# Performance work log

Measured on AMD Instinct MI355X. Metric: run time of the kernel, lower is better.

Reference implementation:

```python
import jax, jax.numpy as jnp
import numpy as np

BN_EPS = 1e-5
L2_EPS = 1e-12

def _conv2d(x, w, pad):
    # x: NCHW, w: OIHW
    return jax.lax.conv_general_dilated(
        x, w, window_strides=(1, 1), padding=[(pad, pad), (pad, pad)],
        dimension_numbers=('NCHW', 'OIHW', 'NCHW'))

def _l2norm(x, axis):
    n = jnp.sqrt(jnp.sum(x * x, axis=axis, keepdims=True))
    return x / jnp.maximum(n, L2_EPS)

def setup_inputs() -> dict:
    key = jax.random.key(0)
    ks = jax.random.split(key, 8)
    x = jax.random.normal(ks[0], (16, 512, 32, 32), dtype=jnp.float32)
    w_proj1 = jax.random.normal(ks[1], (512, 512, 3, 3), dtype=jnp.float32) * 0.02
    bn_gamma = jnp.ones((512,), dtype=jnp.float32)
    bn_beta = jnp.zeros((512,), dtype=jnp.float32)
    bn_mean = jnp.zeros((512,), dtype=jnp.float32)
    bn_var = jnp.ones((512,), dtype=jnp.float32)
    w_proj2 = jax.random.normal(ks[2], (512, 512, 3, 3), dtype=jnp.float32) * 0.02
    w_assign = jax.random.normal(ks[3], (64, 512, 1, 1), dtype=jnp.float32)
    centroids = jax.random.uniform(ks[4], (64, 512), dtype=jnp.float32)
    return {'x': x, 'w_proj1': w_proj1, 'bn_gamma': bn_gamma, 'bn_beta': bn_beta,
            'bn_mean': bn_mean, 'bn_var': bn_var, 'w_proj2': w_proj2,
            'w_assign': w_assign, 'centroids': centroids}

def reference(x, w_proj1, bn_gamma, bn_beta, bn_mean, bn_var, w_proj2, w_assign, centroids):
    # projection head: conv3x3 -> BN (eval) -> ReLU -> conv3x3
    h = _conv2d(x, w_proj1, pad=1)
    inv = jax.lax.rsqrt(bn_var + BN_EPS)
    h = (h - bn_mean[None, :, None, None]) * (bn_gamma * inv)[None, :, None, None] + bn_beta[None, :, None, None]
    h = jax.nn.relu(h)
    x_enc = _conv2d(h, w_proj2, pad=1)

    # descriptor-wise L2 normalization over channels
    xn = _l2norm(x_enc, axis=1)
    N, C, H, W = xn.shape
    K = w_assign.shape[0]

    # soft assignment: 1x1 conv -> softmax over clusters
    sa = _conv2d(xn, w_assign, pad=0).reshape(N, K, H * W)  # [N,K,L]
    sa = jax.nn.softmax(sa, axis=1)

    xf = xn.reshape(N, C, H * W)  # [N,C,L]
    # algebraic rewrite of the per-cluster residual loop:
    # vlad[n,k,c] = sum_l sa[n,k,l]*(xf[n,c,l] - cent[k,c])
    vlad = jnp.einsum('nkl,ncl->nkc', sa, xf) - sa.sum(-1)[:, :, None] * centroids[None]
    vlad = _l2norm(vlad, axis=2)          # intra-normalization
    vlad = vlad.reshape(N, K * C)
    vlad = _l2norm(vlad, axis=1)          # global L2 norm
    return (vlad, x_enc)
```

## Files before the change

kernel.cpp:

```cpp
#include <hip/hip_runtime.h>
#include <math.h>


typedef __bf16 bf16x8 __attribute__((ext_vector_type(8)));
typedef float f32x4 __attribute__((ext_vector_type(4)));

#define GLDS16(gp, lp)                                                  \
  __builtin_amdgcn_global_load_lds(                                     \
      (const __attribute__((address_space(1))) void*)(gp),              \
      (__attribute__((address_space(3))) void*)(lp), 16, 0, 0)

template <int MODE>
__global__ __launch_bounds__(256) void conv_gemm(
    const __bf16* __restrict__ in,
    const __bf16* __restrict__ wt,
    const float* __restrict__ scale, const float* __restrict__ shift,
    __bf16* __restrict__ outp) {
  __shared__ __align__(16) __bf16 Hl[6 * 42 * 64];
  __shared__ __align__(16) __bf16 Wl[2 * 128 * 64];

  const int t = threadIdx.x;
  const int bx = blockIdx.x, oT = blockIdx.y;
  const int lane = t & 63, wid = t >> 6;
  const int l16 = lane & 15, q = lane >> 4;
  const int wrow = wid >> 1, wcol = wid & 1;

  const int n = bx >> 3;
  const int trow0 = (bx & 7) * 4;

  const int swr = t >> 3, sp = t & 7;
  const __bf16* wsrc[4];
#pragma unroll
  for (int i = 0; i < 4; ++i)
    wsrc[i] = wt + (size_t)(oT * 128 + 32 * i + swr) * 4608 + sp * 8;

  const __bf16* inb = in + (size_t)n * (1156 * 512);
  const __bf16* hsrc[8];
  bool hval[8];
#pragma unroll
  for (int i = 0; i < 8; ++i) {
    const int jj = t + 256 * i;
    hval[i] = jj < 2016;
    const int hr = jj / 336;
    const int hrem = jj - hr * 336;
    const int hw = hrem >> 3, hc8 = hrem & 7;
    hsrc[i] = inb + ((size_t)((trow0 + hr) * 34 + hw)) * 512 +
              (hc8 ^ (hw & 7)) * 8;
  }

  const int c0 = (q ^ (l16 & 7)) * 8;
  const int c1 = ((4 + q) ^ (l16 & 7)) * 8;
  int aoff[4], prow_[4], pcol_[4];
#pragma unroll
  for (int i = 0; i < 4; ++i) {
    aoff[i] = (wrow * 64 + i * 16 + l16) * 64;
    const int p = wcol * 64 + i * 16 + l16;
    prow_[i] = p >> 5;
    pcol_[i] = p & 31;
  }

  f32x4 acc[4][4];
#pragma unroll
  for (int i = 0; i < 4; ++i)
#pragma unroll
    for (int j = 0; j < 4; ++j) acc[i][j] = (f32x4){0.f, 0.f, 0.f, 0.f};

#pragma unroll
  for (int i = 0; i < 8; ++i)
    if (hval[i]) GLDS16(hsrc[i], Hl + (t + 256 * i) * 8);
#pragma unroll
  for (int i = 0; i < 4; ++i)
    GLDS16(wsrc[i], Wl + (t + 256 * i) * 8);
#pragma unroll
  for (int i = 0; i < 4; ++i)
    GLDS16(wsrc[i] + 512, Wl + 8192 + (t + 256 * i) * 8);
  asm volatile("s_waitcnt vmcnt(4)" ::: "memory");
  __builtin_amdgcn_s_barrier();

  int tap = 0, dh = 0, dw = 0, cc = 0;
  int tap2 = 2, cc2 = 0;

#pragma unroll 1
  for (int s = 0; s < 72; ++s) {
    const int buf = (s & 1) << 13;
    const __bf16* Wb = Wl + buf;

    bf16x8 aw[4][2], bp[4][2];
#pragma unroll
    for (int i = 0; i < 4; ++i) {
      aw[i][0] = *(const bf16x8*)&Wb[aoff[i] + c0];
      aw[i][1] = *(const bf16x8*)&Wb[aoff[i] + c1];
    }
#pragma unroll
    for (int i = 0; i < 4; ++i) {
      const int col = pcol_[i] + dw;
      const int rb = (prow_[i] + dh) * 2688 + col * 64;
      const int xr = col & 7;
      bp[i][0] = *(const bf16x8*)&Hl[rb + (q ^ xr) * 8];
      bp[i][1] = *(const bf16x8*)&Hl[rb + ((4 + q) ^ xr) * 8];
    }
    asm volatile("s_waitcnt lgkmcnt(0)" ::: "memory");
    __builtin_amdgcn_sched_barrier(0);
    __builtin_amdgcn_s_barrier();

    if (tap == 8 && cc < 7) {
#pragma unroll
      for (int i = 0; i < 8; ++i)
        if (hval[i]) GLDS16(hsrc[i] + (cc + 1) * 64, Hl + (t + 256 * i) * 8);
    }
    if (s < 70) {
      const int woffs2 = (tap2 * 8 + cc2) * 64;
#pragma unroll
      for (int i = 0; i < 4; ++i)
        GLDS16(wsrc[i] + woffs2, Wl + buf + (t + 256 * i) * 8);
    }

    __builtin_amdgcn_s_setprio(1);
#pragma unroll
    for (int kh = 0; kh < 2; ++kh)
#pragma unroll
      for (int mt = 0; mt < 4; ++mt)
#pragma unroll
        for (int nt = 0; nt < 4; ++nt)
          acc[mt][nt] = __builtin_amdgcn_mfma_f32_16x16x32_bf16(
              aw[mt][kh], bp[nt][kh], acc[mt][nt], 0, 0, 0);
    __builtin_amdgcn_s_setprio(0);

    if (s < 70)
      asm volatile("s_waitcnt vmcnt(4)" ::: "memory");
    else
      asm volatile("s_waitcnt vmcnt(0)" ::: "memory");
    __builtin_amdgcn_s_barrier();

    ++tap;
    ++dw;
    if (dw == 3) {
      dw = 0;
      ++dh;
    }
    if (tap == 9) {
      tap = 0;
      dh = 0;
      dw = 0;
      ++cc;
    }
    if (++tap2 == 9) {
      tap2 = 0;
      ++cc2;
    }
  }

#pragma unroll
  for (int nt = 0; nt < 4; ++nt) {
    const int m_l = wcol * 64 + nt * 16 + l16;
    const int mg2 = bx * 128 + m_l;
    const int n2 = mg2 >> 10, pix2 = mg2 & 1023;
#pragma unroll
    for (int mt = 0; mt < 4; ++mt) {
      const int ob = oT * 128 + wrow * 64 + mt * 16 + q * 4;
      f32x4 v = acc[mt][nt];
      union {
        __bf16 b[4];
        uint2 u;
      } pk;
      if (MODE == 0) {
        const f32x4 sc = *(const f32x4*)&scale[ob];
        const f32x4 sh = *(const f32x4*)&shift[ob];
#pragma unroll
        for (int r = 0; r < 4; ++r)
          pk.b[r] = (__bf16)fmaxf(v[r] * sc[r] + sh[r], 0.f);
        __bf16* dst = outp +
                      ((size_t)n2 * 1156 + ((pix2 >> 5) + 1) * 34 +
                       ((pix2 & 31) + 1)) * 512 + ob;
        *(uint2*)dst = pk.u;
      } else {
#pragma unroll
        for (int r = 0; r < 4; ++r) pk.b[r] = (__bf16)v[r];
        __bf16* dst = outp + ((size_t)n2 * 1024 + pix2) * 512 + ob;
        *(uint2*)dst = pk.u;
      }
    }
  }
}

__global__ __launch_bounds__(256) void expand_x(const __bf16* __restrict__ xebT,
                                                float* __restrict__ xenc,
                                                __bf16* __restrict__ xeb) {
  __shared__ __align__(16) __bf16 Ll[64 * 64];
  const int t = threadIdx.x;
  const int cc = blockIdx.x, ptile = blockIdx.y, n = blockIdx.z;
  const int p0 = ptile * 64, c0 = cc * 64;
#pragma unroll
  for (int i = 0; i < 2; ++i) {
    const int u = t * 2 + i;
    const int pix = u >> 3, c8 = u & 7;
    uint4 v =
        *(const uint4*)&xebT[((size_t)n * 1024 + p0 + pix) * 512 + c0 + c8 * 8];
    *(uint4*)&Ll[pix * 64 + (c8 ^ (pix & 7)) * 8] = v;
  }
  __syncthreads();
  const int c = t >> 2, g = t & 3;
  union {
    float f[4];
    float4 v;
  } fv[4];
  union {
    __bf16 b[16];
    uint4 u[2];
  } bv;
#pragma unroll
  for (int r = 0; r < 16; ++r) {
    const int pix = g * 16 + r;
    __bf16 b = Ll[pix * 64 + ((c >> 3) ^ (pix & 7)) * 8 + (c & 7)];
    bv.b[r] = b;
    fv[r >> 2].f[r & 3] = (float)b;
  }
  float* fd = xenc + ((size_t)n * 512 + c0 + c) * 1024 + p0 + g * 16;
#pragma unroll
  for (int r = 0; r < 4; ++r) *(float4*)(fd + r * 4) = fv[r].v;
  __bf16* bd = xeb + ((size_t)n * 512 + c0 + c) * 1024 + p0 + g * 16;
  *(uint4*)bd = bv.u[0];
  *(uint4*)(bd + 8) = bv.u[1];
}

__global__ __launch_bounds__(256) void assign_softmax(
    const __bf16* __restrict__ xebT, const __bf16* __restrict__ watb,
    __bf16* __restrict__ saPb, float* __restrict__ S) {
  __shared__ __align__(16) __bf16 Al[4][64 * 32];
  __shared__ __align__(16) __bf16 Wlb[4][64 * 32];
  __shared__ float Sl[64];
  const int t = threadIdx.x;
  const int pt = blockIdx.x, n = blockIdx.y;
  const int lane = t & 63, wid = t >> 6;
  const int l16 = lane & 15, q = lane >> 4;
  if (t < 64) Sl[t] = 0.f;

  const int arow = t >> 2;
  const __bf16* asrc = xebT + ((size_t)n * 1024 + pt * 64 + arow) * 512 +
                       ((t & 3) ^ ((arow >> 1) & 3)) * 8;
  const __bf16* wsrc = watb + (size_t)(t >> 2) * 512 + (t & 3) * 8;
  const int ldsb = wid * 512;
  const int sw = (q ^ ((l16 >> 1) & 3)) * 8;
  const int pnoff = (t >> 2) * 32 + (t & 3) * 8;

  f32x4 acc[4];
#pragma unroll
  for (int i = 0; i < 4; ++i) acc[i] = (f32x4){0.f, 0.f, 0.f, 0.f};
  float pn = 0.f;

#pragma unroll
  for (int p = 0; p < 3; ++p) {
    GLDS16(asrc + p * 32, (__bf16*)Al[p] + ldsb);
    GLDS16(wsrc + p * 32, (__bf16*)Wlb[p] + ldsb);
  }
  asm volatile("s_waitcnt vmcnt(4)" ::: "memory");
  __builtin_amdgcn_s_barrier();

#pragma unroll 1
  for (int kc = 0; kc < 16; ++kc) {
    const __bf16* Ab = Al[kc & 3];
    const __bf16* Wb = Wlb[kc & 3];
    bf16x8 pv = *(const bf16x8*)&Ab[pnoff];
    bf16x8 pf = *(const bf16x8*)&Ab[(wid * 16 + l16) * 32 + sw];
    bf16x8 wf[4];
#pragma unroll
    for (int ka = 0; ka < 4; ++ka)
      wf[ka] = *(const bf16x8*)&Wb[(ka * 16 + l16) * 32 + sw];
    asm volatile("s_waitcnt lgkmcnt(0)" ::: "memory");
    __builtin_amdgcn_sched_barrier(0);
    __builtin_amdgcn_s_barrier();
    if (kc + 3 < 16) {
      GLDS16(asrc + (kc + 3) * 32, (__bf16*)Al[(kc + 3) & 3] + ldsb);
      GLDS16(wsrc + (kc + 3) * 32, (__bf16*)Wlb[(kc + 3) & 3] + ldsb);
    }
#pragma unroll
    for (int j = 0; j < 8; ++j) {
      float f = (float)pv[j];
      pn = fmaf(f, f, pn);
    }
#pragma unroll
    for (int ka = 0; ka < 4; ++ka)
      acc[ka] =
          __builtin_amdgcn_mfma_f32_16x16x32_bf16(wf[ka], pf, acc[ka], 0, 0, 0);
    if (kc < 13)
      asm volatile("s_waitcnt vmcnt(4)" ::: "memory");
    else
      asm volatile("s_waitcnt vmcnt(0)" ::: "memory");
    __builtin_amdgcn_s_barrier();
  }
  pn += __shfl_xor(pn, 1);
  pn += __shfl_xor(pn, 2);
  const float rn = 1.0f / fmaxf(sqrtf(__shfl(pn, l16 * 4)), 1e-12f);

  float sc[16];
  float m = -3.4e38f;
#pragma unroll
  for (int ka = 0; ka < 4; ++ka)
#pragma unroll
    for (int r = 0; r < 4; ++r) {
      float v = acc[ka][r] * rn;
      sc[ka * 4 + r] = v;
      m = fmaxf(m, v);
    }
  m = fmaxf(m, __shfl_xor(m, 16));
  m = fmaxf(m, __shfl_xor(m, 32));
  float s = 0.f;
#pragma unroll
  for (int j = 0; j < 16; ++j) {
    sc[j] = __expf(sc[j] - m);
    s += sc[j];
  }
  s += __shfl_xor(s, 16);
  s += __shfl_xor(s, 32);
  const float inv = 1.0f / s;
  const int pixg = pt * 64 + wid * 16 + l16;
#pragma unroll
  for (int j = 0; j < 16; ++j) {
    const int k = (j >> 2) * 16 + q * 4 + (j & 3);
    float sa = sc[j] * inv;
    sc[j] = sa;
    saPb[((size_t)n * 64 + k) * 1024 + pixg] = (__bf16)(sa * rn);
  }
#pragma unroll
  for (int j = 0; j < 16; ++j) {
    float v = sc[j];
    v += __shfl_xor(v, 1);
    v += __shfl_xor(v, 2);
    v += __shfl_xor(v, 4);
    v += __shfl_xor(v, 8);
    sc[j] = v;
  }
  if (l16 == 0) {
#pragma unroll
    for (int j = 0; j < 16; ++j)
      atomicAdd(&Sl[(j >> 2) * 16 + q * 4 + (j & 3)], sc[j]);
  }
  __syncthreads();
  if (t < 64) atomicAdd(&S[n * 64 + t], Sl[t]);
}

__global__ __launch_bounds__(256) void vlad_gemm(
    const __bf16* __restrict__ saPb, const __bf16* __restrict__ xeb,
    float* __restrict__ vpart) {
  __shared__ __align__(16) __bf16 Al[4][64 * 32];
  __shared__ __align__(16) __bf16 Bl[4][128 * 32];

  const int t = threadIdx.x;
  const int cT = blockIdx.x, n = blockIdx.y, ks = blockIdx.z;
  const int lane = t & 63, wid = t >> 6;
  const int l16 = lane & 15, q = lane >> 4;
  const int wrow = wid >> 1, wcol = wid & 1;

  const int ar = t >> 2, acp = t & 3;
  const __bf16* asrc = saPb + (size_t)n * 65536 + (size_t)ar * 1024 + ks * 256 +
                       (acp ^ ((ar >> 1) & 3)) * 8;
  const int br0 = t >> 2, bcp0 = t & 3;
  const int br1 = (t + 256) >> 2, bcp1 = t & 3;
  const __bf16* bsrc0 = xeb + (size_t)n * 524288 +
                        (size_t)(cT * 128 + br0) * 1024 + ks * 256 +
                        (bcp0 ^ ((br0 >> 1) & 3)) * 8;
  const __bf16* bsrc1 = xeb + (size_t)n * 524288 +
                        (size_t)(cT * 128 + br1) * 1024 + ks * 256 +
                        (bcp1 ^ ((br1 >> 1) & 3)) * 8;

  const int ldsb = wid * 512;
  const int sw = (q ^ ((l16 >> 1) & 3)) * 8;

  f32x4 acc[2][4];
#pragma unroll
  for (int i = 0; i < 2; ++i)
#pragma unroll
    for (int j = 0; j < 4; ++j) acc[i][j] = (f32x4){0.f, 0.f, 0.f, 0.f};

#pragma unroll
  for (int p = 0; p < 3; ++p) {
    GLDS16(asrc + p * 32, (__bf16*)Al[p] + ldsb);
    GLDS16(bsrc0 + p * 32, (__bf16*)Bl[p] + ldsb);
    GLDS16(bsrc1 + p * 32, (__bf16*)Bl[p] + 2048 + ldsb);
  }
  asm volatile("s_waitcnt vmcnt(6)" ::: "memory");
  __builtin_amdgcn_s_barrier();

#pragma unroll 1
  for (int kc = 0; kc < 8; ++kc) {
    const __bf16* Ab = Al[kc & 3];
    const __bf16* Bb = Bl[kc & 3];
    bf16x8 af[2], bf[4];
#pragma unroll
    for (int i = 0; i < 2; ++i)
      af[i] = *(const bf16x8*)&Ab[(wrow * 32 + i * 16 + l16) * 32 + sw];
#pragma unroll
    for (int i = 0; i < 4; ++i)
      bf[i] = *(const bf16x8*)&Bb[(wcol * 64 + i * 16 + l16) * 32 + sw];
    asm volatile("s_waitcnt lgkmcnt(0)" ::: "memory");
    __builtin_amdgcn_sched_barrier(0);
    __builtin_amdgcn_s_barrier();
    if (kc + 3 < 8) {
      GLDS16(asrc + (kc + 3) * 32, (__bf16*)Al[(kc + 3) & 3] + ldsb);
      GLDS16(bsrc0 + (kc + 3) * 32, (__bf16*)Bl[(kc + 3) & 3] + ldsb);
      GLDS16(bsrc1 + (kc + 3) * 32, (__bf16*)Bl[(kc + 3) & 3] + 2048 + ldsb);
    }
#pragma unroll
    for (int mt = 0; mt < 2; ++mt)
#pragma unroll
      for (int nt = 0; nt < 4; ++nt)
        acc[mt][nt] = __builtin_amdgcn_mfma_f32_16x16x32_bf16(
            af[mt], bf[nt], acc[mt][nt], 0, 0, 0);
    if (kc < 5)
      asm volatile("s_waitcnt vmcnt(6)" ::: "memory");
    else
      asm volatile("s_waitcnt vmcnt(0)" ::: "memory");
    __builtin_amdgcn_s_barrier();
  }

  float* vp = vpart + (size_t)(ks * 16 + n) * 32768;
#pragma unroll
  for (int mt = 0; mt < 2; ++mt) {
    const int krow = wrow * 32 + mt * 16 + q * 4;
#pragma unroll
    for (int nt = 0; nt < 4; ++nt) {
      const int ccol = cT * 128 + wcol * 64 + nt * 16 + l16;
#pragma unroll
      for (int r = 0; r < 4; ++r)
        vp[(size_t)(krow + r) * 512 + ccol] = acc[mt][nt][r];
    }
  }
}

__global__ __launch_bounds__(64) void intra_norm(float* __restrict__ vraw,
                                                 const float* __restrict__ vpart,
                                                 const float* __restrict__ S,
                                                 const float* __restrict__ cent,
                                                 float* __restrict__ gss) {
  const int b = blockIdx.x;
  const int n = b >> 6, k = b & 63;
  const int lane = threadIdx.x;
  const float s = S[b];
  float v[8];
  float ss = 0.f;
#pragma unroll
  for (int j = 0; j < 8; ++j) {
    const int c = lane * 8 + j;
    const size_t off = (size_t)b * 512 + c;
    float val = vpart[off] + vpart[524288 + off] + vpart[2 * 524288 + off] +
                vpart[3 * 524288 + off] - s * cent[k * 512 + c];
    v[j] = val;
    ss += val * val;
  }
#pragma unroll
  for (int off = 1; off < 64; off <<= 1) ss += __shfl_xor(ss, off);
  const float rn = 1.0f / fmaxf(sqrtf(ss), 1e-12f);
#pragma unroll
  for (int j = 0; j < 8; ++j) vraw[(size_t)b * 512 + lane * 8 + j] = v[j] * rn;
  if (lane == 0) atomicAdd(&gss[n], ss * rn * rn);
}

__global__ __launch_bounds__(256) void finalize(const float* __restrict__ vraw,
                                                const float* __restrict__ gss,
                                                float* __restrict__ out) {
  const int id = blockIdx.x * 256 + threadIdx.x;
  const int n = id >> 15;
  out[id] = vraw[id] * (1.0f / fmaxf(sqrtf(gss[n]), 1e-12f));
}

__global__ __launch_bounds__(256) void prep_all(
    const float* __restrict__ x, const float* __restrict__ w1,
    const float* __restrict__ w2, const float* __restrict__ g,
    const float* __restrict__ b, const float* __restrict__ m,
    const float* __restrict__ v, const float* __restrict__ wA,
    __bf16* __restrict__ xpad, __bf16* __restrict__ hpad,
    __bf16* __restrict__ wt1, __bf16* __restrict__ wt2,
    float* __restrict__ scale, float* __restrict__ shift,
    __bf16* __restrict__ watb, float* __restrict__ Sz) {
  __shared__ float Lw[4608];
  const int bx = blockIdx.x;
  const int t = threadIdx.x;

  if (bx < 1056) {
    const int which = bx >= 528;
    const int id = (which ? bx - 528 : bx) * 256 + t;
    const int n = id / 8448;
    const int rem = id - n * 8448;
    const int pb = rem >> 6;
    const int c8 = rem & 63;
    int h, w;
    if (pb < 34) {
      h = 0;
      w = pb;
    } else if (pb < 68) {
      h = 33;
      w = pb - 34;
    } else {
      const int r2 = pb - 68;
      h = 1 + (r2 >> 1);
      w = (r2 & 1) * 33;
    }
    __bf16* base = which ? hpad : xpad;
    *(uint4*)(base + ((size_t)n * 1156 + h * 34 + w) * 512 + c8 * 8) =
        (uint4){0u, 0u, 0u, 0u};
  } else if (bx < 1191) {
    const int i = (bx - 1056) * 256 + t;
    if (i < 512) {
      float sc = g[i] / sqrtf(v[i] + 1e-5f);
      scale[i] = sc;
      shift[i] = b[i] - m[i] * sc;
    } else if (i < 512 + 32768) {
      const int id = i - 512;
      const int k = id >> 9, j = id & 511;
      const int kt = j >> 5, cpos = (j >> 3) & 3, e = j & 7;
      const int c = kt * 32 + (cpos ^ ((k >> 1) & 3)) * 8 + e;
      watb[(size_t)k * 512 + j] = (__bf16)wA[(size_t)k * 512 + c];
    } else if (i < 512 + 32768 + 1040) {
      Sz[i - (512 + 32768)] = 0.f;
    }
  } else if (bx < 1703) {
    const int bb = bx - 1191;
    const int n = bb >> 5, h = bb & 31;
    const int w = t & 31, cg = t >> 5;
    const float* src = x + ((size_t)n * 512 + cg * 64) * 1024 + h * 32 + w;
    __bf16* dst =
        xpad + ((size_t)n * 1156 + (h + 1) * 34 + (w + 1)) * 512 + cg * 64;
    float fv[64];
#pragma unroll
    for (int j = 0; j < 64; ++j) fv[j] = src[j * 1024];
#pragma unroll
    for (int jj = 0; jj < 8; ++jj) {
      union {
        __bf16 b8[8];
        uint4 u;
      } pk;
#pragma unroll
      for (int j = 0; j < 8; ++j) pk.b8[j] = (__bf16)fv[jj * 8 + j];
      *(uint4*)(dst + jj * 8) = pk.u;
    }
  } else {
    const int bb = bx - 1703;
    const int o = bb & 511;
    const float* w = (bb >> 9) ? w2 : w1;
    __bf16* wt = (bb >> 9) ? wt2 : wt1;
#pragma unroll
    for (int i = 0; i < 18; ++i)
      Lw[t + 256 * i] = w[(size_t)o * 4608 + t + 256 * i];
    __syncthreads();
#pragma unroll
    for (int i = 0; i < 18; ++i) {
      const int idk = t + 256 * i;
      const int kt = idk >> 6;
      const int p = (idk >> 3) & 7, e = idk & 7;
      const int logical = p ^ (o & 7);
      const int k2 = kt * 64 + logical * 8 + e;
      const int tap = k2 >> 9, ci = k2 & 511;
      wt[(size_t)o * 4608 + idk] = (__bf16)Lw[ci * 9 + tap];
    }
  }
}

extern "C" void kernel_launch(void* const* d_in, const int* in_sizes, int n_in,
                              void* d_out, int out_size, void* d_ws,
                              size_t ws_size, hipStream_t stream) {
  const float* x = (const float*)d_in[0];
  const float* w1 = (const float*)d_in[1];
  const float* gam = (const float*)d_in[2];
  const float* bet = (const float*)d_in[3];
  const float* mean = (const float*)d_in[4];
  const float* var = (const float*)d_in[5];
  const float* w2 = (const float*)d_in[6];
  const float* wA = (const float*)d_in[7];
  const float* cent = (const float*)d_in[8];
  float* out = (float*)d_out;

  char* ws = (char*)d_ws;
  __bf16* Wt1 = (__bf16*)(ws + 0);
  __bf16* Wt2 = (__bf16*)(ws + 4718592);
  __bf16* xpad = (__bf16*)(ws + 9437184);
  __bf16* xebT = (__bf16*)(ws + 9437184);
  __bf16* saPb = (__bf16*)(ws + 26214400);
  __bf16* hpad = (__bf16*)(ws + 28377088);
  __bf16* xeb = (__bf16*)(ws + 28377088);
  float* vpart = (float*)(ws + 0);
  float* vraw = (float*)(ws + 8388608);
  float* scale = (float*)(ws + 47316992);
  float* shift = (float*)(ws + 47319040);
  __bf16* watb = (__bf16*)(ws + 47321088);
  float* S = (float*)(ws + 47386624);
  float* gss = (float*)(ws + 47390720);

  float* xenc = out + 524288;

  prep_all<<<2727, 256, 0, stream>>>(x, w1, w2, gam, bet, mean, var, wA, xpad,
                                     hpad, Wt1, Wt2, scale, shift, watb, S);

  conv_gemm<0><<<dim3(128, 4), 256, 0, stream>>>(xpad, Wt1, scale, shift, hpad);
  conv_gemm<1><<<dim3(128, 4), 256, 0, stream>>>(hpad, Wt2, nullptr, nullptr,
                                                 xebT);

  expand_x<<<dim3(8, 16, 16), 256, 0, stream>>>(xebT, xenc, xeb);
  assign_softmax<<<dim3(16, 16), 256, 0, stream>>>(xebT, watb, saPb, S);
  vlad_gemm<<<dim3(4, 16, 4), 256, 0, stream>>>(saPb, xeb, vpart);
  intra_norm<<<1024, 64, 0, stream>>>(vraw, vpart, S, cent, gss);
  finalize<<<2048, 256, 0, stream>>>(vraw, gss, out);
}
```

Baseline: 309.6 us.

## Fuse channel-major x_enc output into conv epilogue and split MFMA k-halves

Removes the expand_x kernel: the second conv's epilogue now also writes the fp32 x_enc and bf16 channel-major copies directly, using strided scalar stores. The inner loop is also restructured so the first k-half of MFMAs runs before the LDS barrier, overlapping compute with the remaining LDS reads and the barrier wait. This saves a kernel launch and a global read of xebT, but the epilogue scatter stores are uncoalesced and may cost bandwidth.

```diff
diff --git a/kernel.cpp b/kernel.cpp
--- a/kernel.cpp
+++ b/kernel.cpp
@@ -15,7 +15,8 @@
     const __bf16* __restrict__ in,
     const __bf16* __restrict__ wt,
     const float* __restrict__ scale, const float* __restrict__ shift,
-    __bf16* __restrict__ outp) {
+    __bf16* __restrict__ outp, float* __restrict__ xenc,
+    __bf16* __restrict__ xeb) {
   __shared__ __align__(16) __bf16 Hl[6 * 42 * 64];
   __shared__ __align__(16) __bf16 Wl[2 * 128 * 64];
 
@@ -85,20 +86,32 @@
     const int buf = (s & 1) << 13;
     const __bf16* Wb = Wl + buf;
 
-    bf16x8 aw[4][2], bp[4][2];
-#pragma unroll
-    for (int i = 0; i < 4; ++i) {
-      aw[i][0] = *(const bf16x8*)&Wb[aoff[i] + c0];
-      aw[i][1] = *(const bf16x8*)&Wb[aoff[i] + c1];
-    }
+    bf16x8 aw0[4], aw1[4], bp0[4], bp1[4];
+    int rbs[4], xrs[4];
+#pragma unroll
+    for (int i = 0; i < 4; ++i) aw0[i] = *(const bf16x8*)&Wb[aoff[i] + c0];
 #pragma unroll
     for (int i = 0; i < 4; ++i) {
       const int col = pcol_[i] + dw;
-      const int rb = (prow_[i] + dh) * 2688 + col * 64;
-      const int xr = col & 7;
-      bp[i][0] = *(const bf16x8*)&Hl[rb + (q ^ xr) * 8];
-      bp[i][1] = *(const bf16x8*)&Hl[rb + ((4 + q) ^ xr) * 8];
-    }
+      rbs[i] = (prow_[i] + dh) * 2688 + col * 64;
+      xrs[i] = col & 7;
+      bp0[i] = *(const bf16x8*)&Hl[rbs[i] + (q ^ xrs[i]) * 8];
+    }
+#pragma unroll
+    for (int i = 0; i < 4; ++i) aw1[i] = *(const bf16x8*)&Wb[aoff[i] + c1];
+#pragma unroll
+    for (int i = 0; i < 4; ++i)
+      bp1[i] = *(const bf16x8*)&Hl[rbs[i] + ((4 + q) ^ xrs[i]) * 8];
+
+    __builtin_amdgcn_s_setprio(1);
+#pragma unroll
+    for (int mt = 0; mt < 4; ++mt)
+#pragma unroll
+      for (int nt = 0; nt < 4; ++nt)
+        acc[mt][nt] = __builtin_amdgcn_mfma_f32_16x16x32_bf16(
+            aw0[mt], bp0[nt], acc[mt][nt], 0, 0, 0);
+    __builtin_amdgcn_s_setprio(0);
+
     asm volatile("s_waitcnt lgkmcnt(0)" ::: "memory");
     __builtin_amdgcn_sched_barrier(0);
     __builtin_amdgcn_s_barrier();
@@ -117,13 +130,11 @@
 
     __builtin_amdgcn_s_setprio(1);
 #pragma unroll
-    for (int kh = 0; kh < 2; ++kh)
-#pragma unroll
-      for (int mt = 0; mt < 4; ++mt)
-#pragma unroll
-        for (int nt = 0; nt < 4; ++nt)
-          acc[mt][nt] = __builtin_amdgcn_mfma_f32_16x16x32_bf16(
-              aw[mt][kh], bp[nt][kh], acc[mt][nt], 0, 0, 0);
+    for (int mt = 0; mt < 4; ++mt)
+#pragma unroll
+      for (int nt = 0; nt < 4; ++nt)
+        acc[mt][nt] = __builtin_amdgcn_mfma_f32_16x16x32_bf16(
+            aw1[mt], bp1[nt], acc[mt][nt], 0, 0, 0);
     __builtin_amdgcn_s_setprio(0);
 
     if (s < 70)
@@ -178,49 +189,15 @@
         for (int r = 0; r < 4; ++r) pk.b[r] = (__bf16)v[r];
         __bf16* dst = outp + ((size_t)n2 * 1024 + pix2) * 512 + ob;
         *(uint2*)dst = pk.u;
+        const size_t cb = ((size_t)n2 * 512 + ob) * 1024 + pix2;
+#pragma unroll
+        for (int r = 0; r < 4; ++r) {
+          xenc[cb + (size_t)r * 1024] = v[r];
+          xeb[cb + (size_t)r * 1024] = pk.b[r];
+        }
       }
     }
   }
-}
-
-__global__ __launch_bounds__(256) void expand_x(const __bf16* __restrict__ xebT,
-                                                float* __restrict__ xenc,
-                                                __bf16* __restrict__ xeb) {
-  __shared__ __align__(16) __bf16 Ll[64 * 64];
-  const int t = threadIdx.x;
-  const int cc = blockIdx.x, ptile = blockIdx.y, n = blockIdx.z;
-  const int p0 = ptile * 64, c0 = cc * 64;
-#pragma unroll
-  for (int i = 0; i < 2; ++i) {
-    const int u = t * 2 + i;
-    const int pix = u >> 3, c8 = u & 7;
-    uint4 v =
-        *(const uint4*)&xebT[((size_t)n * 1024 + p0 + pix) * 512 + c0 + c8 * 8];
-    *(uint4*)&Ll[pix * 64 + (c8 ^ (pix & 7)) * 8] = v;
-  }
-  __syncthreads();
-  const int c = t >> 2, g = t & 3;
-  union {
-    float f[4];
-    float4 v;
-  } fv[4];
-  union {
-    __bf16 b[16];
-    uint4 u[2];
-  } bv;
-#pragma unroll
-  for (int r = 0; r < 16; ++r) {
-    const int pix = g * 16 + r;
-    __bf16 b = Ll[pix * 64 + ((c >> 3) ^ (pix & 7)) * 8 + (c & 7)];
-    bv.b[r] = b;
-    fv[r >> 2].f[r & 3] = (float)b;
-  }
-  float* fd = xenc + ((size_t)n * 512 + c0 + c) * 1024 + p0 + g * 16;
-#pragma unroll
-  for (int r = 0; r < 4; ++r) *(float4*)(fd + r * 4) = fv[r].v;
-  __bf16* bd = xeb + ((size_t)n * 512 + c0 + c) * 1024 + p0 + g * 16;
-  *(uint4*)bd = bv.u[0];
-  *(uint4*)(bd + 8) = bv.u[1];
 }
 
 __global__ __launch_bounds__(256) void assign_softmax(
@@ -590,11 +567,11 @@
   prep_all<<<2727, 256, 0, stream>>>(x, w1, w2, gam, bet, mean, var, wA, xpad,
                                      hpad, Wt1, Wt2, scale, shift, watb, S);
 
-  conv_gemm<0><<<dim3(128, 4), 256, 0, stream>>>(xpad, Wt1, scale, shift, hpad);
+  conv_gemm<0><<<dim3(128, 4), 256, 0, stream>>>(xpad, Wt1, scale, shift, hpad,
+                                                 nullptr, nullptr);
   conv_gemm<1><<<dim3(128, 4), 256, 0, stream>>>(hpad, Wt2, nullptr, nullptr,
-                                                 xebT);
-
-  expand_x<<<dim3(8, 16, 16), 256, 0, stream>>>(xebT, xenc, xeb);
+                                                 xebT, xenc, xeb);
+
   assign_softmax<<<dim3(16, 16), 256, 0, stream>>>(xebT, watb, saPb, S);
   vlad_gemm<<<dim3(4, 16, 4), 256, 0, stream>>>(saPb, xeb, vpart);
   intra_norm<<<1024, 64, 0, stream>>>(vraw, vpart, S, cent, gss);
```

New measurement: 319.9 us. 3.3% more time.

## Triple-buffer conv weight tiles, split MFMA k-halves, merge post-conv kernels

Applied to the files above, without the earlier changes.

The conv GEMM main loop now rotates weight tiles through three LDS buffers instead of two. This drops the per-step LDS-read barrier except when the input tile is refilled, and each step's MFMAs are split into two k-halves so the first half can start while the second half's fragments are still loading. Separately, expand_x and assign_softmax are merged into one launch that branches on block index, saving a launch and letting the two run concurrently. The cost is more LDS per block for the conv, which may cut occupancy, and a larger shared-memory footprint for the merged kernel's transpose blocks.

```diff
diff --git a/kernel.cpp b/kernel.cpp
--- a/kernel.cpp
+++ b/kernel.cpp
@@ -17,7 +17,7 @@
     const float* __restrict__ scale, const float* __restrict__ shift,
     __bf16* __restrict__ outp) {
   __shared__ __align__(16) __bf16 Hl[6 * 42 * 64];
-  __shared__ __align__(16) __bf16 Wl[2 * 128 * 64];
+  __shared__ __align__(16) __bf16 Wl[3 * 128 * 64];
 
   const int t = threadIdx.x;
   const int bx = blockIdx.x, oT = blockIdx.y;
@@ -79,51 +79,64 @@
 
   int tap = 0, dh = 0, dw = 0, cc = 0;
   int tap2 = 2, cc2 = 0;
+  int cur = 0;
 
 #pragma unroll 1
   for (int s = 0; s < 72; ++s) {
-    const int buf = (s & 1) << 13;
-    const __bf16* Wb = Wl + buf;
-
-    bf16x8 aw[4][2], bp[4][2];
-#pragma unroll
-    for (int i = 0; i < 4; ++i) {
-      aw[i][0] = *(const bf16x8*)&Wb[aoff[i] + c0];
-      aw[i][1] = *(const bf16x8*)&Wb[aoff[i] + c1];
-    }
+    const __bf16* Wb = Wl + cur * 8192;
+
+    bf16x8 aw0[4], aw1[4], bp0[4], bp1[4];
+    int rbs[4], xrs[4];
+#pragma unroll
+    for (int i = 0; i < 4; ++i) aw0[i] = *(const bf16x8*)&Wb[aoff[i] + c0];
 #pragma unroll
     for (int i = 0; i < 4; ++i) {
       const int col = pcol_[i] + dw;
-      const int rb = (prow_[i] + dh) * 2688 + col * 64;
-      const int xr = col & 7;
-      bp[i][0] = *(const bf16x8*)&Hl[rb + (q ^ xr) * 8];
-      bp[i][1] = *(const bf16x8*)&Hl[rb + ((4 + q) ^ xr) * 8];
-    }
-    asm volatile("s_waitcnt lgkmcnt(0)" ::: "memory");
-    __builtin_amdgcn_sched_barrier(0);
-    __builtin_amdgcn_s_barrier();
-
-    if (tap == 8 && cc < 7) {
-#pragma unroll
-      for (int i = 0; i < 8; ++i)
-        if (hval[i]) GLDS16(hsrc[i] + (cc + 1) * 64, Hl + (t + 256 * i) * 8);
+      rbs[i] = (prow_[i] + dh) * 2688 + col * 64;
+      xrs[i] = col & 7;
+      bp0[i] = *(const bf16x8*)&Hl[rbs[i] + (q ^ xrs[i]) * 8];
+    }
+#pragma unroll
+    for (int i = 0; i < 4; ++i) aw1[i] = *(const bf16x8*)&Wb[aoff[i] + c1];
+#pragma unroll
+    for (int i = 0; i < 4; ++i)
+      bp1[i] = *(const bf16x8*)&Hl[rbs[i] + ((4 + q) ^ xrs[i]) * 8];
+
+    __builtin_amdgcn_s_setprio(1);
+#pragma unroll
+    for (int mt = 0; mt < 4; ++mt)
+#pragma unroll
+      for (int nt = 0; nt < 4; ++nt)
+        acc[mt][nt] = __builtin_amdgcn_mfma_f32_16x16x32_bf16(
+            aw0[mt], bp0[nt], acc[mt][nt], 0, 0, 0);
+    __builtin_amdgcn_s_setprio(0);
+
+    if (tap == 8) {
+      asm volatile("s_waitcnt lgkmcnt(0)" ::: "memory");
+      __builtin_amdgcn_sched_barrier(0);
+      __builtin_amdgcn_s_barrier();
+      if (cc < 7) {
+#pragma unroll
+        for (int i = 0; i < 8; ++i)
+          if (hval[i]) GLDS16(hsrc[i] + (cc + 1) * 64, Hl + (t + 256 * i) * 8);
+      }
     }
     if (s < 70) {
+      int b2 = cur + 2;
+      if (b2 >= 3) b2 -= 3;
       const int woffs2 = (tap2 * 8 + cc2) * 64;
 #pragma unroll
       for (int i = 0; i < 4; ++i)
-        GLDS16(wsrc[i] + woffs2, Wl + buf + (t + 256 * i) * 8);
+        GLDS16(wsrc[i] + woffs2, Wl + b2 * 8192 + (t + 256 * i) * 8);
     }
 
     __builtin_amdgcn_s_setprio(1);
 #pragma unroll
-    for (int kh = 0; kh < 2; ++kh)
-#pragma unroll
-      for (int mt = 0; mt < 4; ++mt)
-#pragma unroll
-        for (int nt = 0; nt < 4; ++nt)
-          acc[mt][nt] = __builtin_amdgcn_mfma_f32_16x16x32_bf16(
-              aw[mt][kh], bp[nt][kh], acc[mt][nt], 0, 0, 0);
+    for (int mt = 0; mt < 4; ++mt)
+#pragma unroll
+      for (int nt = 0; nt < 4; ++nt)
+        acc[mt][nt] = __builtin_amdgcn_mfma_f32_16x16x32_bf16(
+            aw1[mt], bp1[nt], acc[mt][nt], 0, 0, 0);
     __builtin_amdgcn_s_setprio(0);
 
     if (s < 70)
@@ -148,6 +161,7 @@
       tap2 = 0;
       ++cc2;
     }
+    if (++cur == 3) cur = 0;
   }
 
 #pragma unroll
@@ -183,160 +197,161 @@
   }
 }
 
-__global__ __launch_bounds__(256) void expand_x(const __bf16* __restrict__ xebT,
-                                                float* __restrict__ xenc,
-                                                __bf16* __restrict__ xeb) {
-  __shared__ __align__(16) __bf16 Ll[64 * 64];
-  const int t = threadIdx.x;
-  const int cc = blockIdx.x, ptile = blockIdx.y, n = blockIdx.z;
-  const int p0 = ptile * 64, c0 = cc * 64;
-#pragma unroll
-  for (int i = 0; i < 2; ++i) {
-    const int u = t * 2 + i;
-    const int pix = u >> 3, c8 = u & 7;
-    uint4 v =
-        *(const uint4*)&xebT[((size_t)n * 1024 + p0 + pix) * 512 + c0 + c8 * 8];
-    *(uint4*)&Ll[pix * 64 + (c8 ^ (pix & 7)) * 8] = v;
-  }
-  __syncthreads();
-  const int c = t >> 2, g = t & 3;
-  union {
-    float f[4];
-    float4 v;
-  } fv[4];
-  union {
-    __bf16 b[16];
-    uint4 u[2];
-  } bv;
-#pragma unroll
-  for (int r = 0; r < 16; ++r) {
-    const int pix = g * 16 + r;
-    __bf16 b = Ll[pix * 64 + ((c >> 3) ^ (pix & 7)) * 8 + (c & 7)];
-    bv.b[r] = b;
-    fv[r >> 2].f[r & 3] = (float)b;
-  }
-  float* fd = xenc + ((size_t)n * 512 + c0 + c) * 1024 + p0 + g * 16;
-#pragma unroll
-  for (int r = 0; r < 4; ++r) *(float4*)(fd + r * 4) = fv[r].v;
-  __bf16* bd = xeb + ((size_t)n * 512 + c0 + c) * 1024 + p0 + g * 16;
-  *(uint4*)bd = bv.u[0];
-  *(uint4*)(bd + 8) = bv.u[1];
-}
-
-__global__ __launch_bounds__(256) void assign_softmax(
+__global__ __launch_bounds__(256) void post_conv(
     const __bf16* __restrict__ xebT, const __bf16* __restrict__ watb,
-    __bf16* __restrict__ saPb, float* __restrict__ S) {
+    __bf16* __restrict__ saPb, float* __restrict__ S,
+    float* __restrict__ xenc, __bf16* __restrict__ xeb) {
   __shared__ __align__(16) __bf16 Al[4][64 * 32];
   __shared__ __align__(16) __bf16 Wlb[4][64 * 32];
   __shared__ float Sl[64];
   const int t = threadIdx.x;
-  const int pt = blockIdx.x, n = blockIdx.y;
-  const int lane = t & 63, wid = t >> 6;
-  const int l16 = lane & 15, q = lane >> 4;
-  if (t < 64) Sl[t] = 0.f;
-
-  const int arow = t >> 2;
-  const __bf16* asrc = xebT + ((size_t)n * 1024 + pt * 64 + arow) * 512 +
-                       ((t & 3) ^ ((arow >> 1) & 3)) * 8;
-  const __bf16* wsrc = watb + (size_t)(t >> 2) * 512 + (t & 3) * 8;
-  const int ldsb = wid * 512;
-  const int sw = (q ^ ((l16 >> 1) & 3)) * 8;
-  const int pnoff = (t >> 2) * 32 + (t & 3) * 8;
-
-  f32x4 acc[4];
-#pragma unroll
-  for (int i = 0; i < 4; ++i) acc[i] = (f32x4){0.f, 0.f, 0.f, 0.f};
-  float pn = 0.f;
-
-#pragma unroll
-  for (int p = 0; p < 3; ++p) {
-    GLDS16(asrc + p * 32, (__bf16*)Al[p] + ldsb);
-    GLDS16(wsrc + p * 32, (__bf16*)Wlb[p] + ldsb);
-  }
-  asm volatile("s_waitcnt vmcnt(4)" ::: "memory");
-  __builtin_amdgcn_s_barrier();
+  const int bx0 = blockIdx.x;
+
+  if (bx0 < 256) {
+    const int pt = bx0 & 15, n = bx0 >> 4;
+    const int lane = t & 63, wid = t >> 6;
+    const int l16 = lane & 15, q = lane >> 4;
+    if (t < 64) Sl[t] = 0.f;
+
+    const int arow = t >> 2;
+    const __bf16* asrc = xebT + ((size_t)n * 1024 + pt * 64 + arow) * 512 +
+                         ((t & 3) ^ ((arow >> 1) & 3)) * 8;
+    const __bf16* wsrc = watb + (size_t)(t >> 2) * 512 + (t & 3) * 8;
+    const int ldsb = wid * 512;
+    const int sw = (q ^ ((l16 >> 1) & 3)) * 8;
+    const int pnoff = (t >> 2) * 32 + (t & 3) * 8;
+
+    f32x4 acc[4];
+#pragma unroll
+    for (int i = 0; i < 4; ++i) acc[i] = (f32x4){0.f, 0.f, 0.f, 0.f};
+    float pn = 0.f;
+
+#pragma unroll
+    for (int p = 0; p < 3; ++p) {
+      GLDS16(asrc + p * 32, (__bf16*)Al[p] + ldsb);
+      GLDS16(wsrc + p * 32, (__bf16*)Wlb[p] + ldsb);
+    }
+    asm volatile("s_waitcnt vmcnt(4)" ::: "memory");
+    __builtin_amdgcn_s_barrier();
 
 #pragma unroll 1
-  for (int kc = 0; kc < 16; ++kc) {
-    const __bf16* Ab = Al[kc & 3];
-    const __bf16* Wb = Wlb[kc & 3];
-    bf16x8 pv = *(const bf16x8*)&Ab[pnoff];
-    bf16x8 pf = *(const bf16x8*)&Ab[(wid * 16 + l16) * 32 + sw];
-    bf16x8 wf[4];
+    for (int kc = 0; kc < 16; ++kc) {
+      const __bf16* Ab = Al[kc & 3];
+      const __bf16* Wb = Wlb[kc & 3];
+      bf16x8 pv = *(const bf16x8*)&Ab[pnoff];
+      bf16x8 pf = *(const bf16x8*)&Ab[(wid * 16 + l16) * 32 + sw];
+      bf16x8 wf[4];
+#pragma unroll
+      for (int ka = 0; ka < 4; ++ka)
+        wf[ka] = *(const bf16x8*)&Wb[(ka * 16 + l16) * 32 + sw];
+      asm volatile("s_waitcnt lgkmcnt(0)" ::: "memory");
+      __builtin_amdgcn_sched_barrier(0);
+      __builtin_amdgcn_s_barrier();
+      if (kc + 3 < 16) {
+        GLDS16(asrc + (kc + 3) * 32, (__bf16*)Al[(kc + 3) & 3] + ldsb);
+        GLDS16(wsrc + (kc + 3) * 32, (__bf16*)Wlb[(kc + 3) & 3] + ldsb);
+      }
+#pragma unroll
+      for (int j = 0; j < 8; ++j) {
+        float f = (float)pv[j];
+        pn = fmaf(f, f, pn);
+      }
+#pragma unroll
+      for (int ka = 0; ka < 4; ++ka)
+        acc[ka] = __builtin_amdgcn_mfma_f32_16x16x32_bf16(wf[ka], pf, acc[ka],
+                                                          0, 0, 0);
+      if (kc < 13)
+        asm volatile("s_waitcnt vmcnt(4)" ::: "memory");
+      else
+        asm volatile("s_waitcnt vmcnt(0)" ::: "memory");
+      __builtin_amdgcn_s_barrier();
+    }
+    pn += __shfl_xor(pn, 1);
+    pn += __shfl_xor(pn, 2);
+    const float rn = 1.0f / fmaxf(sqrtf(__shfl(pn, l16 * 4)), 1e-12f);
+
+    float sc[16];
+    float m = -3.4e38f;
 #pragma unroll
     for (int ka = 0; ka < 4; ++ka)
-      wf[ka] = *(const bf16x8*)&Wb[(ka * 16 + l16) * 32 + sw];
-    asm volatile("s_waitcnt lgkmcnt(0)" ::: "memory");
-    __builtin_amdgcn_sched_barrier(0);
-    __builtin_amdgcn_s_barrier();
-    if (kc + 3 < 16) {
-      GLDS16(asrc + (kc + 3) * 32, (__bf16*)Al[(kc + 3) & 3] + ldsb);
-      GLDS16(wsrc + (kc + 3) * 32, (__bf16*)Wlb[(kc + 3) & 3] + ldsb);
-    }
-#pragma unroll
-    for (int j = 0; j < 8; ++j) {
-      float f = (float)pv[j];
-      pn = fmaf(f, f, pn);
-    }
-#pragma unroll
-    for (int ka = 0; ka < 4; ++ka)
-      acc[ka] =
-          __builtin_amdgcn_mfma_f32_16x16x32_bf16(wf[ka], pf, acc[ka], 0, 0, 0);
-    if (kc < 13)
-      asm volatile("s_waitcnt vmcnt(4)" ::: "memory");
-    else
-      asm volatile("s_waitcnt vmcnt(0)" ::: "memory");
-    __builtin_amdgcn_s_barrier();
-  }
-  pn += __shfl_xor(pn, 1);
-  pn += __shfl_xor(pn, 2);
-  const float rn = 1.0f / fmaxf(sqrtf(__shfl(pn, l16 * 4)), 1e-12f);
-
-  float sc[16];
-  float m = -3.4e38f;
-#pragma unroll
-  for (int ka = 0; ka < 4; ++ka)
-#pragma unroll
-    for (int r = 0; r < 4; ++r) {
-      float v = acc[ka][r] * rn;
-      sc[ka * 4 + r] = v;
-      m = fmaxf(m, v);
-    }
-  m = fmaxf(m, __shfl_xor(m, 16));
-  m = fmaxf(m, __shfl_xor(m, 32));
-  float s = 0.f;
-#pragma unroll
-  for (int j = 0; j < 16; ++j) {
-    sc[j] = __expf(sc[j] - m);
-    s += sc[j];
-  }
-  s += __shfl_xor(s, 16);
-  s += __shfl_xor(s, 32);
-  const float inv = 1.0f / s;
-  const int pixg = pt * 64 + wid * 16 + l16;
-#pragma unroll
-  for (int j = 0; j < 16; ++j) {
-    const int k = (j >> 2) * 16 + q * 4 + (j & 3);
-    float sa = sc[j] * inv;
-    sc[j] = sa;
-    saPb[((size_t)n * 64 + k) * 1024 + pixg] = (__bf16)(sa * rn);
-  }
-#pragma unroll
-  for (int j = 0; j < 16; ++j) {
-    float v = sc[j];
-    v += __shfl_xor(v, 1);
-    v += __shfl_xor(v, 2);
-    v += __shfl_xor(v, 4);
-    v += __shfl_xor(v, 8);
-    sc[j] = v;
-  }
-  if (l16 == 0) {
-#pragma unroll
-    for (int j = 0; j < 16; ++j)
-      atomicAdd(&Sl[(j >> 2) * 16 + q * 4 + (j & 3)], sc[j]);
-  }
-  __syncthreads();
-  if (t < 64) atomicAdd(&S[n * 64 + t], Sl[t]);
+#pragma unroll
+      for (int r = 0; r < 4; ++r) {
+        float v = acc[ka][r] * rn;
+        sc[ka * 4 + r] = v;
+        m = fmaxf(m, v);
+      }
+    m = fmaxf(m, __shfl_xor(m, 16));
+    m = fmaxf(m, __shfl_xor(m, 32));
+    float s = 0.f;
+#pragma unroll
+    for (int j = 0; j < 16; ++j) {
+      sc[j] = __expf(sc[j] - m);
+      s += sc[j];
+    }
+    s += __shfl_xor(s, 16);
+    s += __shfl_xor(s, 32);
+    const float inv = 1.0f / s;
+    const int pixg = pt * 64 + wid * 16 + l16;
+#pragma unroll
+    for (int j = 0; j < 16; ++j) {
+      const int k = (j >> 2) * 16 + q * 4 + (j & 3);
+      float sa = sc[j] * inv;
+      sc[j] = sa;
+      saPb[((size_t)n * 64 + k) * 1024 + pixg] = (__bf16)(sa * rn);
+    }
+#pragma unroll
+    for (int j = 0; j < 16; ++j) {
+      float v = sc[j];
+      v += __shfl_xor(v, 1);
+      v += __shfl_xor(v, 2);
+      v += __shfl_xor(v, 4);
+      v += __shfl_xor(v, 8);
+      sc[j] = v;
+    }
+    if (l16 == 0) {
+#pragma unroll
+      for (int j = 0; j < 16; ++j)
+        atomicAdd(&Sl[(j >> 2) * 16 + q * 4 + (j & 3)], sc[j]);
+    }
+    __syncthreads();
+    if (t < 64) atomicAdd(&S[n * 64 + t], Sl[t]);
+  } else {
+    const int e = bx0 - 256;
+    const int cc = e & 7, ptile = (e >> 3) & 15, n = e >> 7;
+    __bf16* Ll = (__bf16*)Al;
+    const int p0 = ptile * 64, c0 = cc * 64;
+#pragma unroll
+    for (int i = 0; i < 2; ++i) {
+      const int u = t * 2 + i;
+      const int pix = u >> 3, c8 = u & 7;
+      uint4 v = *(const uint4*)&xebT[((size_t)n * 1024 + p0 + pix) * 512 + c0 +
+                                     c8 * 8];
+      *(uint4*)&Ll[pix * 64 + (c8 ^ (pix & 7)) * 8] = v;
+    }
+    __syncthreads();
+    const int c = t >> 2, g = t & 3;
+    union {
+      float f[4];
+      float4 v;
+    } fv[4];
+    union {
+      __bf16 b[16];
+      uint4 u[2];
+    } bv;
+#pragma unroll
+    for (int r = 0; r < 16; ++r) {
+      const int pix = g * 16 + r;
+      __bf16 b = Ll[pix * 64 + ((c >> 3) ^ (pix & 7)) * 8 + (c & 7)];
+      bv.b[r] = b;
+      fv[r >> 2].f[r & 3] = (float)b;
+    }
+    float* fd = xenc + ((size_t)n * 512 + c0 + c) * 1024 + p0 + g * 16;
+#pragma unroll
+    for (int r = 0; r < 4; ++r) *(float4*)(fd + r * 4) = fv[r].v;
+    __bf16* bd = xeb + ((size_t)n * 512 + c0 + c) * 1024 + p0 + g * 16;
+    *(uint4*)bd = bv.u[0];
+    *(uint4*)(bd + 8) = bv.u[1];
+  }
 }
 
 __global__ __launch_bounds__(256) void vlad_gemm(
@@ -594,8 +609,7 @@
   conv_gemm<1><<<dim3(128, 4), 256, 0, stream>>>(hpad, Wt2, nullptr, nullptr,
                                                  xebT);
 
-  expand_x<<<dim3(8, 16, 16), 256, 0, stream>>>(xebT, xenc, xeb);
-  assign_softmax<<<dim3(16, 16), 256, 0, stream>>>(xebT, watb, saPb, S);
+  post_conv<<<2304, 256, 0, stream>>>(xebT, watb, saPb, S, xenc, xeb);
   vlad_gemm<<<dim3(4, 16, 4), 256, 0, stream>>>(saPb, xeb, vpart);
   intra_norm<<<1024, 64, 0, stream>>>(vraw, vpart, S, cent, gss);
   finalize<<<2048, 256, 0, stream>>>(vraw, gss, out);
```

After: 319.7 us. 1.03x slower.
